# Kernel optimization log

Hardware: AMD Instinct MI355X
Metric: run time of the kernel (lower is better)

The kernel has to match this reference:

```python
import jax, jax.numpy as jnp
import numpy as np
import math

DEPTH = 4
IN_FEATURES = 1024
LEAF_WIDTH = 256
OUT_FEATURES = 1024
BATCH = 8192
N_LEAVES = 2 ** DEPTH      # 16
N_NODES = 2 ** DEPTH - 1   # 15


def setup_inputs() -> dict:
    key = jax.random.key(0)
    ks = jax.random.split(key, 8)
    l1 = 1.0 / math.sqrt(IN_FEATURES)
    l2 = 1.0 / math.sqrt(LEAF_WIDTH)
    u = lambda k, shape, f: jax.random.uniform(k, shape, jnp.float32, -f, f)
    return {
        "x": jax.random.normal(ks[0], (BATCH, IN_FEATURES), jnp.float32),
        "node_weights": u(ks[1], (N_NODES, IN_FEATURES), l1),
        "node_biases": u(ks[2], (N_NODES, 1), l1),
        "w1s": u(ks[3], (N_LEAVES, IN_FEATURES, LEAF_WIDTH), l1),
        "b1s": u(ks[4], (N_LEAVES, LEAF_WIDTH), l1),
        "w2s": u(ks[5], (N_LEAVES, LEAF_WIDTH, OUT_FEATURES), l2),
        "b2s": u(ks[6], (N_LEAVES, OUT_FEATURES), l2),
    }


def reference(x, node_weights, node_biases, w1s, b1s, w2s, b2s):
    # Soft tree-gated routing (training_forward, soft decisions, no leak).
    B = x.shape[0]
    mixture = jnp.ones((B, N_LEAVES), dtype=x.dtype)
    for d in range(DEPTH):  # static small loop over tree depth
        plat, nxt = 2 ** d - 1, 2 ** (d + 1) - 1
        n = 2 ** d
        w = node_weights[plat:nxt]          # (n, F)
        b = node_biases[plat:nxt]           # (n, 1)
        logits = x @ w.T + b.T              # (B, n)
        be = jax.nn.sigmoid(logits)
        # interleave (1-be, be) along node axis -> (B, 2n, 1)
        mod = jnp.stack([1.0 - be, be], axis=-1).reshape(B, 2 * n, 1)
        mixture = (mixture.reshape(B, 2 * n, N_LEAVES // (2 * n)) * mod).reshape(B, N_LEAVES)
    # Per-leaf two-layer MLP, then mixture-weighted sum over leaves.
    h = jnp.einsum("bf,lfh->blh", x, w1s) + b1s[None]          # (B, L, H)
    a = jax.nn.relu(h)
    y = jnp.einsum("blh,lho->blo", a, w2s) + b2s[None]          # (B, L, O)
    return jnp.sum(y * mixture[:, :, None], axis=1)             # (B, O)
```

## Files before the change

kernel.cpp:

```cpp
#include <hip/hip_runtime.h>
#include <hip/hip_bf16.h>
#include <math.h>

#define BATCH 8192
#define INF   1024
#define LEAFW 256
#define OUTF  1024
#define NLEAF 16
#define NNODE 15
#define NTOT  4096
#define KEXT  4160

typedef __bf16 bf16;
typedef __bf16 bf16x4 __attribute__((ext_vector_type(4)));
typedef __bf16 bf16x8 __attribute__((ext_vector_type(8)));
typedef float  f32x4  __attribute__((ext_vector_type(4)));

__global__ __launch_bounds__(256) void prep_weights_kernel(
    const float* __restrict__ w1, const float* __restrict__ w2,
    const float* __restrict__ b2s, bf16* __restrict__ W1T,
    bf16* __restrict__ W2T) {
  __shared__ float tile[32][33];
  int b  = blockIdx.x;
  int t  = threadIdx.x;
  int tx = t & 31, ty = t >> 5;

  if (b < 4096) {
    int l = b >> 8, rem = b & 255;
    int hb = (rem & 7) * 32, fb = (rem >> 3) * 32;
    const float* in1 = w1 + (size_t)l * INF * LEAFW;
#pragma unroll
    for (int i = 0; i < 4; ++i)
      tile[ty + 8 * i][tx] = in1[(size_t)(fb + ty + 8 * i) * LEAFW + hb + tx];
    __syncthreads();
#pragma unroll
    for (int i = 0; i < 4; ++i)
      W1T[(size_t)(l * LEAFW + hb + ty + 8 * i) * INF + fb + tx] =
          (bf16)tile[tx][ty + 8 * i];
  } else if (b < 8192) {
    int bb = b - 4096;
    int l = bb >> 8, rem = bb & 255;
    int ob = (rem & 31) * 32, hb = (rem >> 5) * 32;
    const float* in2 = w2 + (size_t)l * LEAFW * OUTF;
#pragma unroll
    for (int i = 0; i < 4; ++i)
      tile[ty + 8 * i][tx] = in2[(size_t)(hb + ty + 8 * i) * OUTF + ob + tx];
    __syncthreads();
#pragma unroll
    for (int i = 0; i < 4; ++i)
      W2T[(size_t)(ob + ty + 8 * i) * KEXT + l * LEAFW + hb + tx] =
          (bf16)tile[tx][ty + 8 * i];
  } else {
    int i = (b - 8192) * 256 + t;
    int o = i >> 6, j = i & 63;
    W2T[(size_t)o * KEXT + NTOT + j] =
        (j < NLEAF) ? (bf16)b2s[(size_t)j * OUTF + o] : (bf16)0.f;
  }
}

__global__ __launch_bounds__(256) void gating_kernel(
    const float4* __restrict__ x4, const float4* __restrict__ nw4,
    const float* __restrict__ nb, float* __restrict__ mg,
    bf16* __restrict__ Aact, bf16x4* __restrict__ Xbf4) {
  int row  = blockIdx.x * 4 + (threadIdx.x >> 6);
  int lane = threadIdx.x & 63;
  const float4* xr4 = x4 + (size_t)row * (INF / 4);

  float p[NNODE];
#pragma unroll
  for (int j = 0; j < NNODE; ++j) p[j] = 0.f;
#pragma unroll
  for (int c = 0; c < INF / 256; ++c) {
    int idx = c * 64 + lane;
    float4 xv = xr4[idx];
#pragma unroll
    for (int j = 0; j < NNODE; ++j) {
      float4 wv = nw4[j * (INF / 4) + idx];
      p[j] += xv.x * wv.x + xv.y * wv.y + xv.z * wv.z + xv.w * wv.w;
    }
    bf16x4 o = {(bf16)xv.x, (bf16)xv.y, (bf16)xv.z, (bf16)xv.w};
    Xbf4[(size_t)row * (INF / 4) + idx] = o;
  }
#pragma unroll
  for (int j = 0; j < NNODE; ++j) {
    float v = p[j];
#pragma unroll
    for (int off = 32; off > 0; off >>= 1) v += __shfl_xor(v, off);
    p[j] = 1.f / (1.f + expf(-(v + nb[j])));
  }
  float mixv[NLEAF];
#pragma unroll
  for (int L = 0; L < NLEAF; ++L) {
    int n1 = 1 + (L >> 3), n2 = 3 + (L >> 2), n3 = 7 + (L >> 1);
    float m = ((L >> 3) & 1) ? p[0] : (1.f - p[0]);
    m *= ((L >> 2) & 1) ? p[n1] : (1.f - p[n1]);
    m *= ((L >> 1) & 1) ? p[n2] : (1.f - p[n2]);
    m *= (L & 1) ? p[n3] : (1.f - p[n3]);
    mixv[L] = m;
  }
  bf16* arow = Aact + (size_t)row * KEXT + NTOT;
  if (lane == 0) {
#pragma unroll
    for (int L = 0; L < NLEAF; ++L) {
      mg[row * NLEAF + L] = mixv[L];
      arow[L] = (bf16)mixv[L];
    }
  }
  if (lane >= 16) arow[lane] = (bf16)0.f;
}

template <int N>
__device__ __forceinline__ void wait_vmcnt() {
  asm volatile("s_waitcnt vmcnt(%0)" ::"n"(N) : "memory");
}
__device__ __forceinline__ void barrier_fence() {
  asm volatile("" ::: "memory");
  __builtin_amdgcn_s_barrier();
  asm volatile("" ::: "memory");
}

__global__ __launch_bounds__(512, 2) void gemm1_kernel(
    const bf16* __restrict__ A, const bf16* __restrict__ BT,
    const float* __restrict__ bias, const float* __restrict__ mg,
    bf16* __restrict__ outB) {
  constexpr int NT  = INF / 64;
  constexpr int ASZ = 256 * 64;
  constexpr int BSZ = 256 * 64;
  __shared__ __align__(16) bf16 As[2 * ASZ];
  __shared__ __align__(16) bf16 Bs[2 * BSZ];

  const int t = threadIdx.x, lane = t & 63, w = t >> 6;
  const int wm = w >> 2, wn = w & 3;
  const int orig = blockIdx.x;
  const int swz  = (orig & 7) * 64 + (orig >> 3);
  const int bm = (swz >> 4) * 256, bn = (swz & 15) * 256;
  const int lr = t >> 3, cs = t & 7;
  const int scol = ((cs ^ (lr & 7)) << 3);

  auto stageA = [&](int kt, int h, int buf) {
#pragma unroll
    for (int q = 0; q < 2; ++q) {
      const bf16* src =
          A + (size_t)(bm + h * 128 + q * 64 + lr) * INF + kt * 64 + scol;
      __builtin_amdgcn_global_load_lds(
          (const __attribute__((address_space(1))) void*)src,
          (__attribute__((address_space(3))) void*)((char*)As +
                                                    buf * (ASZ * 2) +
                                                    h * 16384 + q * 8192 +
                                                    t * 16),
          16, 0, 0);
    }
  };
  auto stageB = [&](int kt, int h, int buf) {
#pragma unroll
    for (int q = 0; q < 2; ++q) {
      const bf16* src =
          BT + (size_t)(bn + h * 128 + q * 64 + lr) * INF + kt * 64 + scol;
      __builtin_amdgcn_global_load_lds(
          (const __attribute__((address_space(1))) void*)src,
          (__attribute__((address_space(3))) void*)((char*)Bs +
                                                    buf * (BSZ * 2) +
                                                    h * 16384 + q * 8192 +
                                                    t * 16),
          16, 0, 0);
    }
  };
  auto rdA = [&](int buf, int i, int kk) -> bf16x8 {
    int r  = wm * 64 + (i & 3) * 16 + (lane & 15);
    int ch = ((kk << 2) + (lane >> 4)) ^ (lane & 7);
    return *reinterpret_cast<const bf16x8*>(
        &As[buf * ASZ + (i >> 2) * 8192 + r * 64 + ch * 8]);
  };
  auto rdB = [&](int buf, int j, int kk) -> bf16x8 {
    int r  = wn * 32 + (j & 1) * 16 + (lane & 15);
    int ch = ((kk << 2) + (lane >> 4)) ^ (lane & 7);
    return *reinterpret_cast<const bf16x8*>(
        &Bs[buf * BSZ + (j >> 1) * 8192 + r * 64 + ch * 8]);
  };

  f32x4 acc[8][4];
#pragma unroll
  for (int i = 0; i < 8; ++i)
#pragma unroll
    for (int j = 0; j < 4; ++j) acc[i][j] = (f32x4){0.f, 0.f, 0.f, 0.f};

  stageA(0, 0, 0);
  stageB(0, 0, 0);
  stageB(0, 1, 0);
  stageA(0, 1, 0);
  wait_vmcnt<4>();
  barrier_fence();

  for (int kt = 0; kt < NT; ++kt) {
    const int cur = kt & 1, nxt = cur ^ 1;
    const int k1 = kt + 1 < NT ? kt + 1 : NT - 1;
    bf16x8 af0[4][2], af1[4][2], bq0[2][2], bq1[2][2];

#pragma unroll
    for (int i = 0; i < 4; ++i)
#pragma unroll
      for (int kk = 0; kk < 2; ++kk) af0[i][kk] = rdA(cur, i, kk);
#pragma unroll
    for (int j = 0; j < 2; ++j)
#pragma unroll
      for (int kk = 0; kk < 2; ++kk) bq0[j][kk] = rdB(cur, j, kk);
    stageA(k1, 0, nxt);
    __builtin_amdgcn_s_setprio(1);
#pragma unroll
    for (int kk = 0; kk < 2; ++kk)
#pragma unroll
      for (int i = 0; i < 4; ++i)
#pragma unroll
        for (int j = 0; j < 2; ++j)
          acc[i][j] = __builtin_amdgcn_mfma_f32_16x16x32_bf16(
              af0[i][kk], bq0[j][kk], acc[i][j], 0, 0, 0);
    __builtin_amdgcn_s_setprio(0);
    wait_vmcnt<4>();
    barrier_fence();

#pragma unroll
    for (int j = 0; j < 2; ++j)
#pragma unroll
      for (int kk = 0; kk < 2; ++kk) bq1[j][kk] = rdB(cur, 2 + j, kk);
    stageB(k1, 0, nxt);
    __builtin_amdgcn_s_setprio(1);
#pragma unroll
    for (int kk = 0; kk < 2; ++kk)
#pragma unroll
      for (int i = 0; i < 4; ++i)
#pragma unroll
        for (int j = 0; j < 2; ++j)
          acc[i][2 + j] = __builtin_amdgcn_mfma_f32_16x16x32_bf16(
              af0[i][kk], bq1[j][kk], acc[i][2 + j], 0, 0, 0);
    __builtin_amdgcn_s_setprio(0);
    wait_vmcnt<4>();
    barrier_fence();

#pragma unroll
    for (int i = 0; i < 4; ++i)
#pragma unroll
      for (int kk = 0; kk < 2; ++kk) af1[i][kk] = rdA(cur, 4 + i, kk);
    stageB(k1, 1, nxt);
    __builtin_amdgcn_s_setprio(1);
#pragma unroll
    for (int kk = 0; kk < 2; ++kk)
#pragma unroll
      for (int i = 0; i < 4; ++i)
#pragma unroll
        for (int j = 0; j < 2; ++j)
          acc[4 + i][2 + j] = __builtin_amdgcn_mfma_f32_16x16x32_bf16(
              af1[i][kk], bq1[j][kk], acc[4 + i][2 + j], 0, 0, 0);
    __builtin_amdgcn_s_setprio(0);
    wait_vmcnt<6>();
    barrier_fence();

    stageA(k1, 1, nxt);
    __builtin_amdgcn_s_setprio(1);
#pragma unroll
    for (int kk = 0; kk < 2; ++kk)
#pragma unroll
      for (int i = 0; i < 4; ++i)
#pragma unroll
        for (int j = 0; j < 2; ++j)
          acc[4 + i][j] = __builtin_amdgcn_mfma_f32_16x16x32_bf16(
              af1[i][kk], bq0[j][kk], acc[4 + i][j], 0, 0, 0);
    __builtin_amdgcn_s_setprio(0);
    wait_vmcnt<4>();
    barrier_fence();
  }

  const int leaf = bn >> 8;
#pragma unroll
  for (int i = 0; i < 8; ++i) {
    int rb = bm + (i >> 2) * 128 + wm * 64 + (i & 3) * 16 + ((lane >> 4) << 2);
#pragma unroll
    for (int rr = 0; rr < 4; ++rr) {
      const int grow = rb + rr;
      const float g  = mg[grow * NLEAF + leaf];
#pragma unroll
      for (int j = 0; j < 4; ++j) {
        const int gcol =
            bn + (j >> 1) * 128 + wn * 32 + (j & 1) * 16 + (lane & 15);
        float v = acc[i][j][rr] + bias[gcol];
        v = v > 0.f ? v : 0.f;
        outB[(size_t)grow * KEXT + gcol] = (bf16)(v * g);
      }
    }
  }
}

__global__ __launch_bounds__(512, 2) void gemm2_kernel(
    const bf16* __restrict__ A, const bf16* __restrict__ BT,
    float* __restrict__ outF) {
  constexpr int NT  = KEXT / 64;
  constexpr int ASZ = 128 * 64;
  constexpr int BSZ = 256 * 64;
  __shared__ __align__(16) bf16 As[2 * ASZ];
  __shared__ __align__(16) bf16 Bs[2 * BSZ];

  const int t = threadIdx.x, lane = t & 63, w = t >> 6;
  const int wm = w >> 2, wn = w & 3;
  const int orig = blockIdx.x;
  const int swz  = (orig & 7) * 32 + (orig >> 3);
  const int bm = (swz >> 2) * 128, bn = (swz & 3) * 256;
  const int lr = t >> 3, cs = t & 7;
  const int scol = ((cs ^ (lr & 7)) << 3);

  auto stageA = [&](int kt, int buf) {
#pragma unroll
    for (int q = 0; q < 2; ++q) {
      const bf16* src =
          A + (size_t)(bm + q * 64 + lr) * KEXT + kt * 64 + scol;
      __builtin_amdgcn_global_load_lds(
          (const __attribute__((address_space(1))) void*)src,
          (__attribute__((address_space(3))) void*)((char*)As +
                                                    buf * (ASZ * 2) +
                                                    q * 8192 + t * 16),
          16, 0, 0);
    }
  };
  auto stageB = [&](int kt, int h, int buf) {
#pragma unroll
    for (int q = 0; q < 2; ++q) {
      const bf16* src =
          BT + (size_t)(bn + h * 128 + q * 64 + lr) * KEXT + kt * 64 + scol;
      __builtin_amdgcn_global_load_lds(
          (const __attribute__((address_space(1))) void*)src,
          (__attribute__((address_space(3))) void*)((char*)Bs +
                                                    buf * (BSZ * 2) +
                                                    h * 16384 + q * 8192 +
                                                    t * 16),
          16, 0, 0);
    }
  };
  auto rdA = [&](int buf, int i, int kk) -> bf16x8 {
    int r  = (i >> 1) * 64 + wm * 32 + (i & 1) * 16 + (lane & 15);
    int ch = ((kk << 2) + (lane >> 4)) ^ (lane & 7);
    return *reinterpret_cast<const bf16x8*>(
        &As[buf * ASZ + r * 64 + ch * 8]);
  };
  auto rdB = [&](int buf, int j, int kk) -> bf16x8 {
    int r  = wn * 32 + (j & 1) * 16 + (lane & 15);
    int ch = ((kk << 2) + (lane >> 4)) ^ (lane & 7);
    return *reinterpret_cast<const bf16x8*>(
        &Bs[buf * BSZ + (j >> 1) * 8192 + r * 64 + ch * 8]);
  };

  f32x4 acc[4][4];
#pragma unroll
  for (int i = 0; i < 4; ++i)
#pragma unroll
    for (int j = 0; j < 4; ++j) acc[i][j] = (f32x4){0.f, 0.f, 0.f, 0.f};

  stageA(0, 0);
  stageB(0, 0, 0);
  stageB(0, 1, 0);
  wait_vmcnt<2>();
  barrier_fence();

  for (int kt = 0; kt < NT; ++kt) {
    const int cur = kt & 1, nxt = cur ^ 1;
    const int k1 = kt + 1 < NT ? kt + 1 : NT - 1;
    bf16x8 af[4][2], bq0[2][2], bq1[2][2];

#pragma unroll
    for (int i = 0; i < 4; ++i)
#pragma unroll
      for (int kk = 0; kk < 2; ++kk) af[i][kk] = rdA(cur, i, kk);
#pragma unroll
    for (int j = 0; j < 2; ++j)
#pragma unroll
      for (int kk = 0; kk < 2; ++kk) bq0[j][kk] = rdB(cur, j, kk);
    stageA(k1, nxt);
    stageB(k1, 0, nxt);
    __builtin_amdgcn_s_setprio(1);
#pragma unroll
    for (int kk = 0; kk < 2; ++kk)
#pragma unroll
      for (int i = 0; i < 4; ++i)
#pragma unroll
        for (int j = 0; j < 2; ++j)
          acc[i][j] = __builtin_amdgcn_mfma_f32_16x16x32_bf16(
              af[i][kk], bq0[j][kk], acc[i][j], 0, 0, 0);
    __builtin_amdgcn_s_setprio(0);
    wait_vmcnt<4>();
    barrier_fence();

#pragma unroll
    for (int j = 0; j < 2; ++j)
#pragma unroll
      for (int kk = 0; kk < 2; ++kk) bq1[j][kk] = rdB(cur, 2 + j, kk);
    stageB(k1, 1, nxt);
    __builtin_amdgcn_s_setprio(1);
#pragma unroll
    for (int kk = 0; kk < 2; ++kk)
#pragma unroll
      for (int i = 0; i < 4; ++i)
#pragma unroll
        for (int j = 0; j < 2; ++j)
          acc[i][2 + j] = __builtin_amdgcn_mfma_f32_16x16x32_bf16(
              af[i][kk], bq1[j][kk], acc[i][2 + j], 0, 0, 0);
    __builtin_amdgcn_s_setprio(0);
    wait_vmcnt<2>();
    barrier_fence();
  }

#pragma unroll
  for (int i = 0; i < 4; ++i) {
    int rb = bm + (i >> 1) * 64 + wm * 32 + (i & 1) * 16 + ((lane >> 4) << 2);
#pragma unroll
    for (int rr = 0; rr < 4; ++rr) {
      const int grow = rb + rr;
#pragma unroll
      for (int j = 0; j < 4; ++j) {
        const int gcol =
            bn + (j >> 1) * 128 + wn * 32 + (j & 1) * 16 + (lane & 15);
        outF[(size_t)grow * OUTF + gcol] = acc[i][j][rr];
      }
    }
  }
}

extern "C" void kernel_launch(void* const* d_in, const int* in_sizes, int n_in,
                              void* d_out, int out_size, void* d_ws,
                              size_t ws_size, hipStream_t stream) {
  const float* x   = (const float*)d_in[0];
  const float* nw  = (const float*)d_in[1];
  const float* nb  = (const float*)d_in[2];
  const float* w1s = (const float*)d_in[3];
  const float* b1s = (const float*)d_in[4];
  const float* w2s = (const float*)d_in[5];
  const float* b2s = (const float*)d_in[6];
  float* out = (float*)d_out;

  char* ws = (char*)d_ws;
  bf16*  Xbf  = (bf16*)(ws);
  bf16*  W1T  = (bf16*)(ws + 16777216);
  bf16*  W2T  = (bf16*)(ws + 25165824);
  float* mg   = (float*)(ws + 33685504);
  bf16*  Aact = (bf16*)(ws + 34209792);

  prep_weights_kernel<<<dim3(8448), 256, 0, stream>>>(w1s, w2s, b2s, W1T, W2T);
  gating_kernel<<<dim3(BATCH / 4), 256, 0, stream>>>(
      (const float4*)x, (const float4*)nw, nb, mg, Aact, (bf16x4*)Xbf);

  gemm1_kernel<<<dim3(512), 512, 0, stream>>>(Xbf, W1T, b1s, mg, Aact);
  gemm2_kernel<<<dim3(256), 512, 0, stream>>>(Aact, W2T, out);
}
```

Before: 267.3 us.

## Merge weight prep and gating kernels, widen transpose tiles, remap gemm1 blocks

Merges the weight transpose/convert kernel and the gating kernel into a single launch with block ranges selecting the role. The transpose now uses 64x64 tiles with float4 loads and 16-byte bf16x8 stores instead of 32x32 scalar tiles. The gemm1 block-to-tile mapping is changed so each XCD gets a contiguous group of row tiles, aiming for better L2 reuse of A. This saves one launch and improves memory efficiency of the prep, at the risk of LDS bank conflicts on the column-wise tile reads.

```diff
diff --git a/kernel.cpp b/kernel.cpp
--- a/kernel.cpp
+++ b/kernel.cpp
@@ -16,54 +16,71 @@
 typedef __bf16 bf16x8 __attribute__((ext_vector_type(8)));
 typedef float  f32x4  __attribute__((ext_vector_type(4)));
 
-__global__ __launch_bounds__(256) void prep_weights_kernel(
+__global__ __launch_bounds__(256) void prep_gk(
     const float* __restrict__ w1, const float* __restrict__ w2,
-    const float* __restrict__ b2s, bf16* __restrict__ W1T,
-    bf16* __restrict__ W2T) {
-  __shared__ float tile[32][33];
-  int b  = blockIdx.x;
-  int t  = threadIdx.x;
-  int tx = t & 31, ty = t >> 5;
-
-  if (b < 4096) {
-    int l = b >> 8, rem = b & 255;
-    int hb = (rem & 7) * 32, fb = (rem >> 3) * 32;
-    const float* in1 = w1 + (size_t)l * INF * LEAFW;
-#pragma unroll
-    for (int i = 0; i < 4; ++i)
-      tile[ty + 8 * i][tx] = in1[(size_t)(fb + ty + 8 * i) * LEAFW + hb + tx];
+    const float* __restrict__ b2s, const float4* __restrict__ x4,
+    const float4* __restrict__ nw4, const float* __restrict__ nb,
+    bf16* __restrict__ W1T, bf16* __restrict__ W2T, float* __restrict__ mg,
+    bf16* __restrict__ Aact, bf16x4* __restrict__ Xbf4) {
+  __shared__ float tile[64][65];
+  int b = blockIdx.x;
+  int t = threadIdx.x;
+
+  if (b < 2048) {
+    const float* src;
+    bf16* dst;
+    int srcld, dstld, r0, c0;
+    if (b < 1024) {
+      int l = b >> 6, rem = b & 63;
+      r0 = (rem >> 2) * 64;
+      c0 = (rem & 3) * 64;
+      src = w1 + (size_t)l * INF * LEAFW;
+      srcld = LEAFW;
+      dst = W1T + (size_t)l * LEAFW * INF;
+      dstld = INF;
+    } else {
+      int bb = b - 1024;
+      int l = bb >> 6, rem = bb & 63;
+      r0 = (rem >> 4) * 64;
+      c0 = (rem & 15) * 64;
+      src = w2 + (size_t)l * LEAFW * OUTF;
+      srcld = OUTF;
+      dst = W2T + l * LEAFW;
+      dstld = KEXT;
+    }
+    int fr = t >> 4, hc4 = (t & 15) * 4;
+#pragma unroll
+    for (int p = 0; p < 4; ++p) {
+      float4 v = *reinterpret_cast<const float4*>(
+          &src[(size_t)(r0 + fr + p * 16) * srcld + c0 + hc4]);
+      tile[fr + p * 16][hc4 + 0] = v.x;
+      tile[fr + p * 16][hc4 + 1] = v.y;
+      tile[fr + p * 16][hc4 + 2] = v.z;
+      tile[fr + p * 16][hc4 + 3] = v.w;
+    }
     __syncthreads();
 #pragma unroll
-    for (int i = 0; i < 4; ++i)
-      W1T[(size_t)(l * LEAFW + hb + ty + 8 * i) * INF + fb + tx] =
-          (bf16)tile[tx][ty + 8 * i];
-  } else if (b < 8192) {
-    int bb = b - 4096;
-    int l = bb >> 8, rem = bb & 255;
-    int ob = (rem & 31) * 32, hb = (rem >> 5) * 32;
-    const float* in2 = w2 + (size_t)l * LEAFW * OUTF;
-#pragma unroll
-    for (int i = 0; i < 4; ++i)
-      tile[ty + 8 * i][tx] = in2[(size_t)(hb + ty + 8 * i) * OUTF + ob + tx];
-    __syncthreads();
-#pragma unroll
-    for (int i = 0; i < 4; ++i)
-      W2T[(size_t)(ob + ty + 8 * i) * KEXT + l * LEAFW + hb + tx] =
-          (bf16)tile[tx][ty + 8 * i];
-  } else {
-    int i = (b - 8192) * 256 + t;
+    for (int p = 0; p < 2; ++p) {
+      int s = t + p * 256;
+      int h = s >> 3, fc = (s & 7) * 8;
+      bf16x8 o;
+#pragma unroll
+      for (int e = 0; e < 8; ++e) o[e] = (bf16)tile[fc + e][h];
+      *reinterpret_cast<bf16x8*>(&dst[(size_t)(c0 + h) * dstld + r0 + fc]) = o;
+    }
+    return;
+  }
+
+  if (b < 2304) {
+    int i = (b - 2048) * 256 + t;
     int o = i >> 6, j = i & 63;
     W2T[(size_t)o * KEXT + NTOT + j] =
         (j < NLEAF) ? (bf16)b2s[(size_t)j * OUTF + o] : (bf16)0.f;
-  }
-}
-
-__global__ __launch_bounds__(256) void gating_kernel(
-    const float4* __restrict__ x4, const float4* __restrict__ nw4,
-    const float* __restrict__ nb, float* __restrict__ mg,
-    bf16* __restrict__ Aact, bf16x4* __restrict__ Xbf4) {
-  int row  = blockIdx.x * 4 + (threadIdx.x >> 6);
-  int lane = threadIdx.x & 63;
+    return;
+  }
+
+  int row  = (b - 2304) * 4 + (t >> 6);
+  int lane = t & 63;
   const float4* xr4 = x4 + (size_t)row * (INF / 4);
 
   float p[NNODE];
@@ -132,8 +149,9 @@
   const int t = threadIdx.x, lane = t & 63, w = t >> 6;
   const int wm = w >> 2, wn = w & 3;
   const int orig = blockIdx.x;
-  const int swz  = (orig & 7) * 64 + (orig >> 3);
-  const int bm = (swz >> 4) * 256, bn = (swz & 15) * 256;
+  const int xcd  = orig & 7, idx = orig >> 3;
+  const int bm = ((xcd << 2) + (idx & 3)) * 256;
+  const int bn = (idx >> 2) * 256;
   const int lr = t >> 3, cs = t & 7;
   const int scol = ((cs ^ (lr & 7)) << 3);
 
@@ -309,8 +327,7 @@
   auto stageA = [&](int kt, int buf) {
 #pragma unroll
     for (int q = 0; q < 2; ++q) {
-      const bf16* src =
-          A + (size_t)(bm + q * 64 + lr) * KEXT + kt * 64 + scol;
+      const bf16* src = A + (size_t)(bm + q * 64 + lr) * KEXT + kt * 64 + scol;
       __builtin_amdgcn_global_load_lds(
           (const __attribute__((address_space(1))) void*)src,
           (__attribute__((address_space(3))) void*)((char*)As +
@@ -336,8 +353,7 @@
   auto rdA = [&](int buf, int i, int kk) -> bf16x8 {
     int r  = (i >> 1) * 64 + wm * 32 + (i & 1) * 16 + (lane & 15);
     int ch = ((kk << 2) + (lane >> 4)) ^ (lane & 7);
-    return *reinterpret_cast<const bf16x8*>(
-        &As[buf * ASZ + r * 64 + ch * 8]);
+    return *reinterpret_cast<const bf16x8*>(&As[buf * ASZ + r * 64 + ch * 8]);
   };
   auto rdB = [&](int buf, int j, int kk) -> bf16x8 {
     int r  = wn * 32 + (j & 1) * 16 + (lane & 15);
@@ -440,9 +456,9 @@
   float* mg   = (float*)(ws + 33685504);
   bf16*  Aact = (bf16*)(ws + 34209792);
 
-  prep_weights_kernel<<<dim3(8448), 256, 0, stream>>>(w1s, w2s, b2s, W1T, W2T);
-  gating_kernel<<<dim3(BATCH / 4), 256, 0, stream>>>(
-      (const float4*)x, (const float4*)nw, nb, mg, Aact, (bf16x4*)Xbf);
+  prep_gk<<<dim3(4352), 256, 0, stream>>>(
+      w1s, w2s, b2s, (const float4*)x, (const float4*)nw, nb, W1T, W2T, mg,
+      Aact, (bf16x4*)Xbf);
 
   gemm1_kernel<<<dim3(512), 512, 0, stream>>>(Xbf, W1T, b1s, mg, Aact);
   gemm2_kernel<<<dim3(256), 512, 0, stream>>>(Aact, W2T, out);
```

Result: no change. 264.0 us (-1.3%).
